# Performance work log

Measured on AMD Instinct MI355X. Metric: run time of the kernel, lower is better.

## Reference

```python
import jax, jax.numpy as jnp
import numpy as np

N0, N1, N2 = 100000, 20000, 4000   # src(block0), dst(block0)=src(block1), dst(block1)
R = 3                               # number of relations
E0, E1 = 160000, 64000              # edges per relation per block
IN_FEATS, HID = 128, 128
TSS, RS = 64, 64
NTOT = 200000                       # global node count for tss/rs embed tables
F_IN = HID + TSS + RS               # IGConv input feature dim = 256


def _lin(key, fi, fo):
    k1, k2 = jax.random.split(key)
    s = float(1.0 / np.sqrt(fi))
    w = jax.random.uniform(k1, (fi, fo), minval=-s, maxval=s, dtype=jnp.float32)
    b = jax.random.uniform(k2, (fo,), minval=-s, maxval=s, dtype=jnp.float32)
    return w, b


def setup_inputs() -> dict:
    ks = jax.random.split(jax.random.key(0), 32)
    inp = {}
    inp["x_user"] = jax.random.normal(ks[0], (N0, IN_FEATS), dtype=jnp.float32)
    inp["tss_embed"] = jax.random.normal(ks[1], (NTOT, TSS), dtype=jnp.float32)
    inp["rs_embed"] = jax.random.normal(ks[2], (NTOT, RS), dtype=jnp.float32)
    inp["src_nid0"] = jax.random.randint(ks[3], (N0,), 0, NTOT)
    inp["src_nid1"] = jax.random.randint(ks[4], (N1,), 0, NTOT)
    inp["e0_src"] = jax.random.randint(ks[5], (R, E0), 0, N0)
    inp["e0_dst"] = jax.random.randint(ks[6], (R, E0), 0, N1)
    inp["e1_src"] = jax.random.randint(ks[7], (R, E1), 0, N1)
    inp["e1_dst"] = jax.random.randint(ks[8], (R, E1), 0, N2)
    inp["embed_w"], inp["embed_b"] = _lin(ks[9], IN_FEATS, HID)
    i = 10
    for l in (1, 2):
        for nm, fi in (("fc1", F_IN), ("fc2", 3 * F_IN), ("fc3", 2 * HID)):
            pw, pb = zip(*[_lin(jax.random.fold_in(ks[i], r), fi, HID) for r in range(R)])
            inp["l%d_%s_w" % (l, nm)] = jnp.stack(pw)  # [R, fi, HID]
            inp["l%d_%s_b" % (l, nm)] = jnp.stack(pb)  # [R, HID]
            i += 1
    inp["attn_w1"], inp["attn_b1"] = _lin(ks[i], HID, HID)
    inp["attn_w2"] = _lin(ks[i + 1], HID, 1)[0]  # Linear(hid,1,bias=False)
    inp["pred_w"], inp["pred_b"] = _lin(ks[i + 2], HID, 1)
    return inp


def _igconv(src_feat, dst_feat, esrc, edst, n_dst, fc1w, fc1b, fc2w, fc2b, fc3w, fc3b):
    # copy_u gather then max/mean/sum segment reductions over destination nodes
    m = src_feat[esrc]                                   # [E, F]
    s = jax.ops.segment_sum(m, edst, num_segments=n_dst)
    deg = jax.ops.segment_sum(jnp.ones(esrc.shape, m.dtype), edst, num_segments=n_dst)
    mean = s / jnp.maximum(deg, 1.0)[:, None]
    mx = jax.ops.segment_max(m, edst, num_segments=n_dst)
    mx = jnp.where(deg[:, None] > 0, mx, jnp.zeros_like(mx))  # DGL zeros for isolated dst
    msg = jnp.concatenate([mx, mean, s], axis=1)         # [n_dst, 3F]
    inp = jnp.concatenate([msg @ fc2w + fc2b, dst_feat @ fc1w + fc1b], axis=1)
    return jax.nn.relu(inp) @ fc3w + fc3b                # [n_dst, HID]


def _attn(z, w1, b1, w2):
    # SemanticAttention: z [N, R, HID]
    w = (jnp.tanh(z @ w1 + b1) @ w2).mean(0)             # [R, 1]
    beta = jax.nn.softmax(w, axis=0)                     # [R, 1]
    return (beta[None] * z).sum(1)                       # [N, HID]


def _forward(x_user, tss_embed, rs_embed, embed_w, embed_b,
             l1_fc1_w, l1_fc1_b, l1_fc2_w, l1_fc2_b, l1_fc3_w, l1_fc3_b,
             l2_fc1_w, l2_fc1_b, l2_fc2_w, l2_fc2_b, l2_fc3_w, l2_fc3_b,
             attn_w1, attn_b1, attn_w2, pred_w, pred_b,
             src_nid0, src_nid1, e0_src, e0_dst, e1_src, e1_dst):
    u0 = x_user @ embed_w + embed_b                      # self.embed
    feat0 = jnp.concatenate([u0, tss_embed[src_nid0], rs_embed[src_nid0]], axis=1)  # [N0,256]
    conv1 = jax.vmap(lambda es, ed, w1, b1, w2, b2, w3, b3:
                     _igconv(feat0, feat0[:N1], es, ed, N1, w1, b1, w2, b2, w3, b3))
    z1 = conv1(e0_src, e0_dst, l1_fc1_w, l1_fc1_b, l1_fc2_w, l1_fc2_b, l1_fc3_w, l1_fc3_b)  # [R,N1,HID]
    h1 = jax.nn.relu(_attn(jnp.transpose(z1, (1, 0, 2)), attn_w1, attn_b1, attn_w2))  # [N1,HID]
    feat1 = jnp.concatenate([h1, tss_embed[src_nid1], rs_embed[src_nid1]], axis=1)    # [N1,256]
    conv2 = jax.vmap(lambda es, ed, w1, b1, w2, b2, w3, b3:
                     _igconv(feat1, feat1[:N2], es, ed, N2, w1, b1, w2, b2, w3, b3))
    z2 = conv2(e1_src, e1_dst, l2_fc1_w, l2_fc1_b, l2_fc2_w, l2_fc2_b, l2_fc3_w, l2_fc3_b)  # [R,N2,HID]
    h2 = _attn(jnp.transpose(z2, (1, 0, 2)), attn_w1, attn_b1, attn_w2)              # [N2,HID]
    return jax.nn.sigmoid(h2 @ pred_w + pred_b)          # [N2,1]


def reference(x_user, tss_embed, rs_embed, src_nid0, src_nid1,
              e0_src, e0_dst, e1_src, e1_dst, embed_w, embed_b,
              l1_fc1_w, l1_fc1_b, l1_fc2_w, l1_fc2_b, l1_fc3_w, l1_fc3_b,
              l2_fc1_w, l2_fc1_b, l2_fc2_w, l2_fc2_b, l2_fc3_w, l2_fc3_b,
              attn_w1, attn_b1, attn_w2, pred_w, pred_b):
    return _forward(x_user, tss_embed, rs_embed, embed_w, embed_b,
                    l1_fc1_w, l1_fc1_b, l1_fc2_w, l1_fc2_b, l1_fc3_w, l1_fc3_b,
                    l2_fc1_w, l2_fc1_b, l2_fc2_w, l2_fc2_b, l2_fc3_w, l2_fc3_b,
                    attn_w1, attn_b1, attn_w2, pred_w, pred_b,
                    src_nid0, src_nid1, e0_src, e0_dst, e1_src, e1_dst)
```

## Files before the change

kernel.cpp:

```cpp
#include <hip/hip_runtime.h>
#include <math.h>


typedef short s16x8 __attribute__((ext_vector_type(8)));
typedef float f32x4 __attribute__((ext_vector_type(4)));

__device__ __forceinline__ ushort f2bf(float f) {
  unsigned u = __float_as_uint(f);
  return (ushort)((u + 0x7FFFu + ((u >> 16) & 1u)) >> 16);
}
__device__ __forceinline__ float bf2f(unsigned hbits) {
  return __uint_as_float(hbits << 16);
}
__device__ __forceinline__ unsigned pack2(float lo, float hi) {
  return (unsigned)f2bf(lo) | ((unsigned)f2bf(hi) << 16);
}

struct PrepAll {
  const float* src[8];
  ushort* dst[8];
  int K[8];
  int total[8];
};

__global__ __launch_bounds__(256) void prep_all(PrepAll P)
{
  int t = blockIdx.z;
  int off = blockIdx.x * 256 + threadIdx.x;
  if (off >= P.total[t]) return;
  int K = P.K[t];
  int k = off % K;
  int n = (off / K) & 127;
  int r = off / (K * 128);
  P.dst[t][off] = f2bf(P.src[t][((size_t)r * K + k) * 128 + n]);
}

struct GemmDesc {
  const void* A; int lda; size_t aStride; int aKind;
  const ushort* Wt; size_t wStride;
  const float* bias; int biasStride;
  void* C; int ldc; size_t cStride; int cKind;
  int M, K, relu;
  const ushort* aggM; const ushort* aggS; const float* invdeg;
  size_t aggStride; int invStride;
  const int* gnid; const float* gtss; const float* grs;
};

__global__ __launch_bounds__(256) void gemm_mfma(GemmDesc d0, GemmDesc d1)
{
  const GemmDesc d = blockIdx.z ? d1 : d0;
  const int r = blockIdx.y;
  __shared__ __align__(16) ushort Bs[2048 * 8];

  const int tid = threadIdx.x;
  const int wave = tid >> 6, lane = tid & 63;
  const int m16 = lane & 15, quad = lane >> 4;
  const int rowBase = blockIdx.x * 64;
  const int row = rowBase + wave * 16 + m16;
  const bool rowOK = row < d.M;
  const ushort* Wt = d.Wt + (size_t)r * d.wStride;

  f32x4 acc[8];
  #pragma unroll
  for (int j = 0; j < 8; ++j)
    #pragma unroll
    for (int p = 0; p < 4; ++p) acc[j][p] = 0.f;

  float idg = 1.f;
  if (d.aKind == 2 && rowOK) idg = d.invdeg[(size_t)r * d.invStride + row];

  const ushort* Ab16 = (const ushort*)d.A + (size_t)r * d.aStride;
  const float*  Ab32 = (const float*)d.A + (size_t)r * d.aStride;

  for (int c0 = 0; c0 < d.K; c0 += 128) {
    if (c0) __syncthreads();
    #pragma unroll
    for (int i = 0; i < 8; ++i) {
      int q = tid + 256 * i;
      int col = ((q >> 6) & 7) * 16 + (q & 15);
      int kk  = c0 + (q >> 9) * 32 + ((q >> 4) & 3) * 8;
      *(uint4*)&Bs[q * 8] = *(const uint4*)(Wt + (size_t)col * d.K + kk);
    }
    __syncthreads();

    #pragma unroll
    for (int ks = 0; ks < 4; ++ks) {
      const int k0 = c0 + ks * 32;
      uint4 pk = make_uint4(0u, 0u, 0u, 0u);
      if (rowOK) {
        if (d.aKind == 1) {
          pk = *(const uint4*)(Ab16 + (size_t)row * d.lda + k0 + quad * 8);
        } else if (d.aKind == 0) {
          float4 fa = *(const float4*)(Ab32 + (size_t)row * d.lda + k0 + quad * 8);
          float4 fb = *(const float4*)(Ab32 + (size_t)row * d.lda + k0 + quad * 8 + 4);
          pk.x = pack2(fa.x, fa.y); pk.y = pack2(fa.z, fa.w);
          pk.z = pack2(fb.x, fb.y); pk.w = pack2(fb.z, fb.w);
        } else {
          int seg = k0 >> 8;
          int jj  = (k0 & 255) + quad * 8;
          const ushort* Ag = (seg == 0 ? d.aggM : d.aggS) + (size_t)r * d.aggStride;
          pk = *(const uint4*)(Ag + (size_t)row * 256 + jj);
          if (seg == 1) {
            pk.x = pack2(bf2f(pk.x & 0xFFFFu) * idg, bf2f(pk.x >> 16) * idg);
            pk.y = pack2(bf2f(pk.y & 0xFFFFu) * idg, bf2f(pk.y >> 16) * idg);
            pk.z = pack2(bf2f(pk.z & 0xFFFFu) * idg, bf2f(pk.z >> 16) * idg);
            pk.w = pack2(bf2f(pk.w & 0xFFFFu) * idg, bf2f(pk.w >> 16) * idg);
          }
        }
      }
      s16x8 af = *(s16x8*)&pk;
      #pragma unroll
      for (int j = 0; j < 8; ++j) {
        s16x8 bf = *(const s16x8*)&Bs[((ks * 8 + j) * 64 + lane) * 8];
        acc[j] = __builtin_amdgcn_mfma_f32_16x16x32_bf16(af, bf, acc[j], 0, 0, 0);
      }
    }
  }

  const float* bias = d.bias + (size_t)r * d.biasStride;
  float bcol[8];
  #pragma unroll
  for (int j = 0; j < 8; ++j) bcol[j] = bias[j * 16 + m16];

  #pragma unroll
  for (int p = 0; p < 4; ++p) {
    int grow = rowBase + wave * 16 + quad * 4 + p;
    if (grow >= d.M) continue;
    if (d.cKind == 0) {
      float* Crow = (float*)d.C + (size_t)r * d.cStride + (size_t)grow * d.ldc;
      #pragma unroll
      for (int j = 0; j < 8; ++j) {
        float v = acc[j][p] + bcol[j];
        if (d.relu) v = fmaxf(v, 0.f);
        Crow[j * 16 + m16] = v;
      }
    } else {
      ushort* Crow = (ushort*)d.C + (size_t)r * d.cStride + (size_t)grow * d.ldc;
      #pragma unroll
      for (int j = 0; j < 8; ++j) {
        float v = acc[j][p] + bcol[j];
        if (d.relu) v = fmaxf(v, 0.f);
        Crow[j * 16 + m16] = f2bf(v);
      }
    }
  }

  if (d.gnid) {
    #pragma unroll
    for (int i = 0; i < 8; ++i) {
      int q = tid + 256 * i;
      int grow = rowBase + (q >> 5);
      int c = q & 31;
      if (grow >= d.M) continue;
      int id = d.gnid[grow];
      float4 v = (c < 16) ? *(const float4*)(d.gtss + (size_t)id * 64 + c * 4)
                          : *(const float4*)(d.grs  + (size_t)id * 64 + (c - 16) * 4);
      uint2 g; g.x = pack2(v.x, v.y); g.y = pack2(v.z, v.w);
      *(uint2*)((ushort*)d.C + (size_t)grow * d.ldc + 128 + c * 4) = g;
    }
  }
}

__global__ __launch_bounds__(256) void attn_mfma(
    const float* __restrict__ z, const ushort* __restrict__ w1t,
    const float* __restrict__ b1, const float* __restrict__ w2,
    int N, float* __restrict__ wsum)
{
  const int r = blockIdx.y;
  const float* zr = z + (size_t)r * N * 128;
  __shared__ __align__(16) ushort Bs[2048 * 8];

  const int tid = threadIdx.x;
  const int wave = tid >> 6, lane = tid & 63;
  const int m16 = lane & 15, quad = lane >> 4;
  const int rowBase = blockIdx.x * 64;
  const int row = rowBase + wave * 16 + m16;
  const bool rowOK = row < N;

  f32x4 acc[8];
  #pragma unroll
  for (int j = 0; j < 8; ++j)
    #pragma unroll
    for (int p = 0; p < 4; ++p) acc[j][p] = 0.f;

  #pragma unroll
  for (int i = 0; i < 8; ++i) {
    int q = tid + 256 * i;
    int col = ((q >> 6) & 7) * 16 + (q & 15);
    int kk  = (q >> 9) * 32 + ((q >> 4) & 3) * 8;
    *(uint4*)&Bs[q * 8] = *(const uint4*)(w1t + (size_t)col * 128 + kk);
  }
  __syncthreads();

  #pragma unroll
  for (int ks = 0; ks < 4; ++ks) {
    const int k0 = ks * 32;
    uint4 pk = make_uint4(0u, 0u, 0u, 0u);
    if (rowOK) {
      float4 fa = *(const float4*)(zr + (size_t)row * 128 + k0 + quad * 8);
      float4 fb = *(const float4*)(zr + (size_t)row * 128 + k0 + quad * 8 + 4);
      pk.x = pack2(fa.x, fa.y); pk.y = pack2(fa.z, fa.w);
      pk.z = pack2(fb.x, fb.y); pk.w = pack2(fb.z, fb.w);
    }
    s16x8 af = *(s16x8*)&pk;
    #pragma unroll
    for (int j = 0; j < 8; ++j) {
      s16x8 bf = *(const s16x8*)&Bs[((ks * 8 + j) * 64 + lane) * 8];
      acc[j] = __builtin_amdgcn_mfma_f32_16x16x32_bf16(af, bf, acc[j], 0, 0, 0);
    }
  }

  float b1c[8], w2c[8];
  #pragma unroll
  for (int j = 0; j < 8; ++j) { b1c[j] = b1[j * 16 + m16]; w2c[j] = w2[j * 16 + m16]; }

  float local = 0.f;
  #pragma unroll
  for (int p = 0; p < 4; ++p) {
    int grow = rowBase + wave * 16 + quad * 4 + p;
    if (grow >= N) continue;
    #pragma unroll
    for (int j = 0; j < 8; ++j)
      local += tanhf(acc[j][p] + b1c[j]) * w2c[j];
  }
  #pragma unroll
  for (int o = 32; o > 0; o >>= 1) local += __shfl_down(local, o);
  __shared__ float red[4];
  if (lane == 0) red[wave] = local;
  __syncthreads();
  if (tid == 0) atomicAdd(&wsum[r], red[0] + red[1] + red[2] + red[3]);
}

__global__ void count_deg(const int* __restrict__ edst, int E, int N, int* __restrict__ deg)
{
  int e = blockIdx.x * blockDim.x + threadIdx.x;
  int r = blockIdx.y;
  if (e < E) atomicAdd(&deg[r * N + edst[(size_t)r * E + e]], 1);
}

__global__ __launch_bounds__(1024) void scan_kernel(
    const int* __restrict__ deg, int* __restrict__ rowptr,
    int* __restrict__ cursor, int N)
{
  __shared__ int wtot[16];
  __shared__ int chunk_total_s;
  const int tid = threadIdx.x, lane = tid & 63, wid = tid >> 6;
  int running = 0;
  for (int base = 0; base < N; base += 4096) {
    int i0 = base + tid * 4;
    int d0 = 0, d1 = 0, d2 = 0, d3 = 0;
    if (i0 < N) {
      if (i0 + 3 < N) { int4 t = *(const int4*)(deg + i0); d0 = t.x; d1 = t.y; d2 = t.z; d3 = t.w; }
      else { d0 = deg[i0]; if (i0+1 < N) d1 = deg[i0+1]; if (i0+2 < N) d2 = deg[i0+2]; }
    }
    int tsum = d0 + d1 + d2 + d3;
    int incl = tsum;
    #pragma unroll
    for (int o = 1; o < 64; o <<= 1) {
      int t = __shfl_up(incl, o);
      if (lane >= o) incl += t;
    }
    if (lane == 63) wtot[wid] = incl;
    __syncthreads();
    if (wid == 0 && lane < 16) {
      int t = wtot[lane];
      int inc = t;
      #pragma unroll
      for (int o = 1; o < 16; o <<= 1) {
        int u = __shfl_up(inc, o);
        if (lane >= o) inc += u;
      }
      wtot[lane] = inc - t;
      if (lane == 15) chunk_total_s = inc;
    }
    __syncthreads();
    int excl = running + wtot[wid] + (incl - tsum);
    if (i0 < N) {
      int e1 = excl + d0, e2 = e1 + d1, e3 = e2 + d2;
      if (i0 + 3 < N) {
        *(int4*)(rowptr + i0) = make_int4(excl, e1, e2, e3);
        *(int4*)(cursor + i0) = make_int4(0, 0, 0, 0);
      } else {
        rowptr[i0] = excl; cursor[i0] = 0;
        if (i0+1 < N) { rowptr[i0+1] = e1; cursor[i0+1] = 0; }
        if (i0+2 < N) { rowptr[i0+2] = e2; cursor[i0+2] = 0; }
      }
    }
    running += chunk_total_s;
    __syncthreads();
  }
  if (tid == 0) rowptr[N] = running;
}

__global__ void fill_csr(const int* __restrict__ esrc, const int* __restrict__ edst,
                         int E, int N, const int* __restrict__ rowptr,
                         int* __restrict__ cursor, int* __restrict__ csr)
{
  int e = blockIdx.x * blockDim.x + threadIdx.x;
  int r = blockIdx.y;
  if (e >= E) return;
  int d = r * N + edst[(size_t)r * E + e];
  int pos = atomicAdd(&cursor[d], 1);
  csr[rowptr[d] + pos] = esrc[(size_t)r * E + e];
}

__global__ __launch_bounds__(256) void agg_kernel(
    const ushort* __restrict__ feat, const int* __restrict__ csr,
    const int* __restrict__ rowptr, int N, int c0, int cr, int CH,
    ushort* __restrict__ aggS, ushort* __restrict__ aggM, float* __restrict__ invdeg)
{
  const int wid = threadIdx.x >> 6, lane = threadIdx.x & 63;
  const int node = blockIdx.x * 4 + wid;
  if (node >= cr) return;
  const int g = blockIdx.y * N + c0 + node;
  const int o = blockIdx.y * CH + node;
  const int start = rowptr[g], end = rowptr[g + 1];
  const int j = lane * 4;
  float s0 = 0.f, s1 = 0.f, s2 = 0.f, s3 = 0.f;
  float m0 = -INFINITY, m1 = -INFINITY, m2 = -INFINITY, m3 = -INFINITY;
  int e = start;
  for (; e + 4 <= end; e += 4) {
    int sa = csr[e], sb = csr[e+1], sc = csr[e+2], sd = csr[e+3];
    uint2 va = *(const uint2*)(feat + (size_t)sa * 256 + j);
    uint2 vb = *(const uint2*)(feat + (size_t)sb * 256 + j);
    uint2 vc = *(const uint2*)(feat + (size_t)sc * 256 + j);
    uint2 vd = *(const uint2*)(feat + (size_t)sd * 256 + j);
    float a0, a1, a2, a3;
    a0 = bf2f(va.x & 0xFFFFu); a1 = bf2f(va.x >> 16); a2 = bf2f(va.y & 0xFFFFu); a3 = bf2f(va.y >> 16);
    s0 += a0; s1 += a1; s2 += a2; s3 += a3;
    m0 = fmaxf(m0, a0); m1 = fmaxf(m1, a1); m2 = fmaxf(m2, a2); m3 = fmaxf(m3, a3);
    a0 = bf2f(vb.x & 0xFFFFu); a1 = bf2f(vb.x >> 16); a2 = bf2f(vb.y & 0xFFFFu); a3 = bf2f(vb.y >> 16);
    s0 += a0; s1 += a1; s2 += a2; s3 += a3;
    m0 = fmaxf(m0, a0); m1 = fmaxf(m1, a1); m2 = fmaxf(m2, a2); m3 = fmaxf(m3, a3);
    a0 = bf2f(vc.x & 0xFFFFu); a1 = bf2f(vc.x >> 16); a2 = bf2f(vc.y & 0xFFFFu); a3 = bf2f(vc.y >> 16);
    s0 += a0; s1 += a1; s2 += a2; s3 += a3;
    m0 = fmaxf(m0, a0); m1 = fmaxf(m1, a1); m2 = fmaxf(m2, a2); m3 = fmaxf(m3, a3);
    a0 = bf2f(vd.x & 0xFFFFu); a1 = bf2f(vd.x >> 16); a2 = bf2f(vd.y & 0xFFFFu); a3 = bf2f(vd.y >> 16);
    s0 += a0; s1 += a1; s2 += a2; s3 += a3;
    m0 = fmaxf(m0, a0); m1 = fmaxf(m1, a1); m2 = fmaxf(m2, a2); m3 = fmaxf(m3, a3);
  }
  for (; e < end; ++e) {
    int src = csr[e];
    uint2 v = *(const uint2*)(feat + (size_t)src * 256 + j);
    float a0 = bf2f(v.x & 0xFFFFu), a1 = bf2f(v.x >> 16);
    float a2 = bf2f(v.y & 0xFFFFu), a3 = bf2f(v.y >> 16);
    s0 += a0; s1 += a1; s2 += a2; s3 += a3;
    m0 = fmaxf(m0, a0); m1 = fmaxf(m1, a1); m2 = fmaxf(m2, a2); m3 = fmaxf(m3, a3);
  }
  if (end == start) { m0 = m1 = m2 = m3 = 0.f; }
  uint2 ps; ps.x = pack2(s0, s1); ps.y = pack2(s2, s3);
  *(uint2*)(aggS + (size_t)o * 256 + j) = ps;
  uint2 pm; pm.x = pack2(m0, m1); pm.y = pack2(m2, m3);
  *(uint2*)(aggM + (size_t)o * 256 + j) = pm;
  if (lane == 0) invdeg[o] = 1.f / fmaxf((float)(end - start), 1.f);
}

__global__ void beta_kernel(const float* __restrict__ wsum, float invN, float* __restrict__ beta) {
  float w0 = wsum[0] * invN, w1 = wsum[1] * invN, w2 = wsum[2] * invN;
  float m  = fmaxf(w0, fmaxf(w1, w2));
  float e0 = expf(w0 - m), e1 = expf(w1 - m), e2 = expf(w2 - m);
  float s  = e0 + e1 + e2;
  beta[0] = e0 / s; beta[1] = e1 / s; beta[2] = e2 / s;
}

__global__ __launch_bounds__(256) void combine1_kernel(
    const float* __restrict__ z1, const float* __restrict__ beta,
    const float* __restrict__ tss, const float* __restrict__ rs,
    const int* __restrict__ nid, int N, ushort* __restrict__ feat1)
{
  int n = blockIdx.x, t = threadIdx.x;
  size_t NH = (size_t)N * 128;
  if (t < 128) {
    float v = beta[0] * z1[(size_t)n*128 + t] + beta[1] * z1[NH + (size_t)n*128 + t]
            + beta[2] * z1[2*NH + (size_t)n*128 + t];
    feat1[(size_t)n*256 + t] = f2bf(fmaxf(v, 0.f));
  } else {
    int j = t - 128;
    int id = nid[n];
    float v = (j < 64) ? tss[(size_t)id*64 + j] : rs[(size_t)id*64 + j - 64];
    feat1[(size_t)n*256 + t] = f2bf(v);
  }
}

__global__ __launch_bounds__(128) void combine2_pred(
    const float* __restrict__ z2, const float* __restrict__ beta, int N,
    const float* __restrict__ pw, const float* __restrict__ pb, float* __restrict__ out)
{
  int n = blockIdx.x, t = threadIdx.x;
  size_t NH = (size_t)N * 128;
  float h = beta[0] * z2[(size_t)n*128 + t] + beta[1] * z2[NH + (size_t)n*128 + t]
          + beta[2] * z2[2*NH + (size_t)n*128 + t];
  float p = h * pw[t];
  #pragma unroll
  for (int o = 32; o > 0; o >>= 1) p += __shfl_down(p, o);
  __shared__ float red[2];
  if ((t & 63) == 0) red[t >> 6] = p;
  __syncthreads();
  if (t == 0) {
    float v = red[0] + red[1] + pb[0];
    out[n] = 1.f / (1.f + expf(-v));
  }
}

extern "C" void kernel_launch(void* const* d_in, const int* in_sizes, int n_in,
                              void* d_out, int out_size, void* d_ws, size_t ws_size,
                              hipStream_t stream)
{
  const float* x_user  = (const float*)d_in[0];
  const float* tss     = (const float*)d_in[1];
  const float* rs      = (const float*)d_in[2];
  const int* src_nid0  = (const int*)d_in[3];
  const int* src_nid1  = (const int*)d_in[4];
  const int* e0_src    = (const int*)d_in[5];
  const int* e0_dst    = (const int*)d_in[6];
  const int* e1_src    = (const int*)d_in[7];
  const int* e1_dst    = (const int*)d_in[8];
  const float* embed_w = (const float*)d_in[9];
  const float* embed_b = (const float*)d_in[10];
  const float* l1w[3]  = {(const float*)d_in[11], (const float*)d_in[13], (const float*)d_in[15]};
  const float* l1b[3]  = {(const float*)d_in[12], (const float*)d_in[14], (const float*)d_in[16]};
  const float* l2w[3]  = {(const float*)d_in[17], (const float*)d_in[19], (const float*)d_in[21]};
  const float* l2b[3]  = {(const float*)d_in[18], (const float*)d_in[20], (const float*)d_in[22]};
  const float* attn_w1 = (const float*)d_in[23];
  const float* attn_b1 = (const float*)d_in[24];
  const float* attn_w2 = (const float*)d_in[25];
  const float* pred_w  = (const float*)d_in[26];
  const float* pred_b  = (const float*)d_in[27];
  float* out = (float*)d_out;

  const int N0 = in_sizes[0] / 128;
  const int N1 = in_sizes[4];
  const int N2 = out_size;
  const int E0 = in_sizes[5] / 3;
  const int E1 = in_sizes[7] / 3;

  char* wp = (char*)d_ws;
  auto walloc = [&](size_t bytes) {
    char* p = wp; wp += (bytes + 255) & ~(size_t)255; return p;
  };
  ushort* feat0  = (ushort*)walloc((size_t)N0 * 256 * 2);
  ushort* inp    = (ushort*)walloc((size_t)3 * N1 * 256 * 2);
  float*  z      = (float*)walloc((size_t)3 * N1 * 128 * 4);
  ushort* wt_emb = (ushort*)walloc((size_t)128 * 128 * 2);
  ushort* wt_attn = (ushort*)walloc((size_t)128 * 128 * 2);
  ushort* wt_fc1[2], *wt_fc2[2], *wt_fc3[2];
  for (int l = 0; l < 2; ++l) {
    wt_fc1[l] = (ushort*)walloc((size_t)3 * 256 * 128 * 2);
    wt_fc2[l] = (ushort*)walloc((size_t)3 * 768 * 128 * 2);
    wt_fc3[l] = (ushort*)walloc((size_t)3 * 256 * 128 * 2);
  }
  int*   degcnt = (int*)walloc((size_t)3 * N1 * 4);
  int*   rowptr = (int*)walloc((size_t)(3 * N1 + 1) * 4);
  int*   csr    = (int*)walloc((size_t)3 * E0 * 4);
  float* small  = (float*)walloc(256);
  float* wsum = small;
  float* beta = small + 4;
  ushort* feat1 = feat0;

  size_t used = (size_t)(wp - (char*)d_ws);
  size_t avail = (ws_size > used + 65536) ? (ws_size - used - 65536) : 0;
  const size_t per_row = (size_t)3 * (2 * 256 * 2 + 4 + 64);
  int CH = (int)(avail / per_row);
  if (CH > N1) CH = N1;
  if (CH < 1024) CH = 1024;
  ushort* aggS   = (ushort*)walloc((size_t)3 * CH * 256 * 2);
  ushort* aggM   = (ushort*)walloc((size_t)3 * CH * 256 * 2);
  float*  invdeg = (float*)walloc((size_t)3 * CH * 4);
  (void)n_in;

  {
    PrepAll P;
    P.src[0] = embed_w;  P.dst[0] = wt_emb;    P.K[0] = 128; P.total[0] = 128 * 128;
    P.src[1] = attn_w1;  P.dst[1] = wt_attn;   P.K[1] = 128; P.total[1] = 128 * 128;
    P.src[2] = l1w[0];   P.dst[2] = wt_fc1[0]; P.K[2] = 256; P.total[2] = 3 * 256 * 128;
    P.src[3] = l1w[1];   P.dst[3] = wt_fc2[0]; P.K[3] = 768; P.total[3] = 3 * 768 * 128;
    P.src[4] = l1w[2];   P.dst[4] = wt_fc3[0]; P.K[4] = 256; P.total[4] = 3 * 256 * 128;
    P.src[5] = l2w[0];   P.dst[5] = wt_fc1[1]; P.K[5] = 256; P.total[5] = 3 * 256 * 128;
    P.src[6] = l2w[1];   P.dst[6] = wt_fc2[1]; P.K[6] = 768; P.total[6] = 3 * 768 * 128;
    P.src[7] = l2w[2];   P.dst[7] = wt_fc3[1]; P.K[7] = 256; P.total[7] = 3 * 256 * 128;
    prep_all<<<dim3((3 * 768 * 128 + 255) / 256, 1, 8), 256, 0, stream>>>(P);
  }

  GemmDesc dz = {};

  {
    GemmDesc d{};
    d.A = x_user; d.lda = 128; d.aStride = 0; d.aKind = 0;
    d.Wt = wt_emb; d.wStride = 0; d.bias = embed_b; d.biasStride = 0;
    d.C = feat0; d.ldc = 256; d.cStride = 0; d.cKind = 1;
    d.M = N0; d.K = 128; d.relu = 0;
    d.aggM = aggM; d.aggS = aggS; d.invdeg = invdeg; d.aggStride = 0; d.invStride = 0;
    d.gnid = src_nid0; d.gtss = tss; d.grs = rs;
    gemm_mfma<<<dim3((N0 + 63) / 64, 1, 1), 256, 0, stream>>>(d, dz);
  }

  for (int layer = 0; layer < 2; ++layer) {
    const ushort* featS = layer ? feat1 : feat0;
    int Nd = layer ? N2 : N1;
    int E  = layer ? E1 : E0;
    const int* es = layer ? e1_src : e0_src;
    const int* ed = layer ? e1_dst : e0_dst;
    const float* const* lb = layer ? l2b : l1b;

    hipMemsetAsync(degcnt, 0, (size_t)3 * Nd * 4, stream);
    count_deg<<<dim3((E + 255) / 256, 3), 256, 0, stream>>>(ed, E, Nd, degcnt);
    scan_kernel<<<1, 1024, 0, stream>>>(degcnt, rowptr, degcnt, 3 * Nd);
    fill_csr<<<dim3((E + 255) / 256, 3), 256, 0, stream>>>(es, ed, E, Nd, rowptr, degcnt, csr);

    for (int c0 = 0; c0 < Nd; c0 += CH) {
      int cr = (Nd - c0 < CH) ? (Nd - c0) : CH;
      agg_kernel<<<dim3((cr + 3) / 4, 3), 256, 0, stream>>>(
          featS, csr, rowptr, Nd, c0, cr, CH, aggS, aggM, invdeg);
      GemmDesc d2{};
      d2.A = nullptr; d2.lda = 0; d2.aStride = 0; d2.aKind = 2;
      d2.Wt = wt_fc2[layer]; d2.wStride = (size_t)768 * 128; d2.bias = lb[1]; d2.biasStride = 128;
      d2.C = inp + (size_t)c0 * 256; d2.ldc = 256; d2.cStride = (size_t)Nd * 256; d2.cKind = 1;
      d2.M = cr; d2.K = 768; d2.relu = 1;
      d2.aggM = aggM; d2.aggS = aggS; d2.invdeg = invdeg;
      d2.aggStride = (size_t)CH * 256; d2.invStride = CH;
      GemmDesc d1{};
      d1.A = featS + (size_t)c0 * 256; d1.lda = 256; d1.aStride = 0; d1.aKind = 1;
      d1.Wt = wt_fc1[layer]; d1.wStride = (size_t)256 * 128; d1.bias = lb[0]; d1.biasStride = 128;
      d1.C = inp + 128 + (size_t)c0 * 256; d1.ldc = 256; d1.cStride = (size_t)Nd * 256; d1.cKind = 1;
      d1.M = cr; d1.K = 256; d1.relu = 1;
      d1.aggM = aggM; d1.aggS = aggS; d1.invdeg = invdeg; d1.aggStride = 0; d1.invStride = 0;
      gemm_mfma<<<dim3((cr + 63) / 64, 3, 2), 256, 0, stream>>>(d2, d1);
    }
    {
      GemmDesc d3{};
      d3.A = inp; d3.lda = 256; d3.aStride = (size_t)N1 * 0 + (size_t)Nd * 256; d3.aKind = 1;
      d3.Wt = wt_fc3[layer]; d3.wStride = (size_t)256 * 128; d3.bias = lb[2]; d3.biasStride = 128;
      d3.C = z; d3.ldc = 128; d3.cStride = (size_t)Nd * 128; d3.cKind = 0;
      d3.M = Nd; d3.K = 256; d3.relu = 0;
      d3.aggM = aggM; d3.aggS = aggS; d3.invdeg = invdeg; d3.aggStride = 0; d3.invStride = 0;
      gemm_mfma<<<dim3((Nd + 63) / 64, 3, 1), 256, 0, stream>>>(d3, dz);
    }

    hipMemsetAsync(wsum, 0, 3 * sizeof(float), stream);
    attn_mfma<<<dim3((Nd + 63) / 64, 3), 256, 0, stream>>>(z, wt_attn, attn_b1, attn_w2, Nd, wsum);
    beta_kernel<<<1, 1, 0, stream>>>(wsum, 1.0f / (float)Nd, beta);

    if (layer == 0) {
      combine1_kernel<<<N1, 256, 0, stream>>>(z, beta, tss, rs, src_nid1, N1, feat1);
    } else {
      combine2_pred<<<N2, 128, 0, stream>>>(z, beta, N2, pred_w, pred_b, out);
    }
  }
}
```

Before: 546.8 us.

## Template GEMM on K and A-kind, halve LDS tile, prefetch A fragments

The GEMM kernel is specialised by a template on K and on how A is loaded, which removes the runtime branches on aKind. The shared-memory B tile shrinks from 128 to 64 K-columns per stage, halving LDS use so more blocks fit per CU, and launch bounds now request 4 blocks per SM. A fragments are loaded into registers ahead of the B staging: all of them up front when K is at most 256, otherwise per chunk. The attention kernel gets the same change. The cost is more __syncthreads barriers and higher register pressure from the prefetched fragments.

```diff
diff --git a/kernel.cpp b/kernel.cpp
--- a/kernel.cpp
+++ b/kernel.cpp
@@ -46,11 +46,42 @@
   const int* gnid; const float* gtss; const float* grs;
 };
 
-__global__ __launch_bounds__(256) void gemm_mfma(GemmDesc d0, GemmDesc d1)
-{
-  const GemmDesc d = blockIdx.z ? d1 : d0;
-  const int r = blockIdx.y;
-  __shared__ __align__(16) ushort Bs[2048 * 8];
+template<int AKIND>
+__device__ __forceinline__ uint4 loadA(const void* Ab, const ushort* AgM,
+                                       const ushort* AgS, int lda, int row,
+                                       bool rowOK, int k0, int quad, float idg)
+{
+  uint4 pk = make_uint4(0u, 0u, 0u, 0u);
+  if (rowOK) {
+    if constexpr (AKIND == 1) {
+      pk = *(const uint4*)((const ushort*)Ab + (size_t)row * lda + k0 + quad * 8);
+    } else if constexpr (AKIND == 0) {
+      const float* A32 = (const float*)Ab;
+      float4 fa = *(const float4*)(A32 + (size_t)row * lda + k0 + quad * 8);
+      float4 fb = *(const float4*)(A32 + (size_t)row * lda + k0 + quad * 8 + 4);
+      pk.x = pack2(fa.x, fa.y); pk.y = pack2(fa.z, fa.w);
+      pk.z = pack2(fb.x, fb.y); pk.w = pack2(fb.z, fb.w);
+    } else {
+      int seg = k0 >> 8;
+      int jj  = (k0 & 255) + quad * 8;
+      const ushort* Ag = (seg == 0) ? AgM : AgS;
+      pk = *(const uint4*)(Ag + (size_t)row * 256 + jj);
+      if (seg == 1) {
+        pk.x = pack2(bf2f(pk.x & 0xFFFFu) * idg, bf2f(pk.x >> 16) * idg);
+        pk.y = pack2(bf2f(pk.y & 0xFFFFu) * idg, bf2f(pk.y >> 16) * idg);
+        pk.z = pack2(bf2f(pk.z & 0xFFFFu) * idg, bf2f(pk.z >> 16) * idg);
+        pk.w = pack2(bf2f(pk.w & 0xFFFFu) * idg, bf2f(pk.w >> 16) * idg);
+      }
+    }
+  }
+  return pk;
+}
+
+template<int K, int AKIND>
+__device__ __forceinline__ void gemm_core(const GemmDesc& d, int r, ushort* Bs)
+{
+  constexpr int NC = K / 64;
+  constexpr int NF = K / 32;
 
   const int tid = threadIdx.x;
   const int wave = tid >> 6, lane = tid & 63;
@@ -60,54 +91,46 @@
   const bool rowOK = row < d.M;
   const ushort* Wt = d.Wt + (size_t)r * d.wStride;
 
+  const void* Ab = (const char*)d.A +
+      (size_t)r * d.aStride * (AKIND == 0 ? sizeof(float) : sizeof(ushort));
+  const ushort* AgM = d.aggM + (size_t)r * d.aggStride;
+  const ushort* AgS = d.aggS + (size_t)r * d.aggStride;
+
+  float idg = 1.f;
+  if (AKIND == 2 && rowOK) idg = d.invdeg[(size_t)r * d.invStride + row];
+
   f32x4 acc[8];
   #pragma unroll
   for (int j = 0; j < 8; ++j)
     #pragma unroll
     for (int p = 0; p < 4; ++p) acc[j][p] = 0.f;
 
-  float idg = 1.f;
-  if (d.aKind == 2 && rowOK) idg = d.invdeg[(size_t)r * d.invStride + row];
-
-  const ushort* Ab16 = (const ushort*)d.A + (size_t)r * d.aStride;
-  const float*  Ab32 = (const float*)d.A + (size_t)r * d.aStride;
-
-  for (int c0 = 0; c0 < d.K; c0 += 128) {
-    if (c0) __syncthreads();
-    #pragma unroll
-    for (int i = 0; i < 8; ++i) {
+  uint4 pkAll[(K <= 256) ? NF : 2];
+  if constexpr (K <= 256) {
+    #pragma unroll
+    for (int f = 0; f < NF; ++f)
+      pkAll[f] = loadA<AKIND>(Ab, AgM, AgS, d.lda, row, rowOK, f * 32, quad, idg);
+  }
+
+  #pragma unroll
+  for (int c = 0; c < NC; ++c) {
+    if constexpr (K > 256) {
+      pkAll[0] = loadA<AKIND>(Ab, AgM, AgS, d.lda, row, rowOK, c * 64,      quad, idg);
+      pkAll[1] = loadA<AKIND>(Ab, AgM, AgS, d.lda, row, rowOK, c * 64 + 32, quad, idg);
+    }
+    if (c) __syncthreads();
+    #pragma unroll
+    for (int i = 0; i < 4; ++i) {
       int q = tid + 256 * i;
       int col = ((q >> 6) & 7) * 16 + (q & 15);
-      int kk  = c0 + (q >> 9) * 32 + ((q >> 4) & 3) * 8;
-      *(uint4*)&Bs[q * 8] = *(const uint4*)(Wt + (size_t)col * d.K + kk);
+      int kk  = c * 64 + (q >> 9) * 32 + ((q >> 4) & 3) * 8;
+      *(uint4*)&Bs[q * 8] = *(const uint4*)(Wt + (size_t)col * K + kk);
     }
     __syncthreads();
 
     #pragma unroll
-    for (int ks = 0; ks < 4; ++ks) {
-      const int k0 = c0 + ks * 32;
-      uint4 pk = make_uint4(0u, 0u, 0u, 0u);
-      if (rowOK) {
-        if (d.aKind == 1) {
-          pk = *(const uint4*)(Ab16 + (size_t)row * d.lda + k0 + quad * 8);
-        } else if (d.aKind == 0) {
-          float4 fa = *(const float4*)(Ab32 + (size_t)row * d.lda + k0 + quad * 8);
-          float4 fb = *(const float4*)(Ab32 + (size_t)row * d.lda + k0 + quad * 8 + 4);
-          pk.x = pack2(fa.x, fa.y); pk.y = pack2(fa.z, fa.w);
-          pk.z = pack2(fb.x, fb.y); pk.w = pack2(fb.z, fb.w);
-        } else {
-          int seg = k0 >> 8;
-          int jj  = (k0 & 255) + quad * 8;
-          const ushort* Ag = (seg == 0 ? d.aggM : d.aggS) + (size_t)r * d.aggStride;
-          pk = *(const uint4*)(Ag + (size_t)row * 256 + jj);
-          if (seg == 1) {
-            pk.x = pack2(bf2f(pk.x & 0xFFFFu) * idg, bf2f(pk.x >> 16) * idg);
-            pk.y = pack2(bf2f(pk.y & 0xFFFFu) * idg, bf2f(pk.y >> 16) * idg);
-            pk.z = pack2(bf2f(pk.z & 0xFFFFu) * idg, bf2f(pk.z >> 16) * idg);
-            pk.w = pack2(bf2f(pk.w & 0xFFFFu) * idg, bf2f(pk.w >> 16) * idg);
-          }
-        }
-      }
+    for (int ks = 0; ks < 2; ++ks) {
+      uint4 pk = (K <= 256) ? pkAll[c * 2 + ks] : pkAll[ks];
       s16x8 af = *(s16x8*)&pk;
       #pragma unroll
       for (int j = 0; j < 8; ++j) {
@@ -145,30 +168,42 @@
     }
   }
 
-  if (d.gnid) {
-    #pragma unroll
-    for (int i = 0; i < 8; ++i) {
-      int q = tid + 256 * i;
-      int grow = rowBase + (q >> 5);
-      int c = q & 31;
-      if (grow >= d.M) continue;
-      int id = d.gnid[grow];
-      float4 v = (c < 16) ? *(const float4*)(d.gtss + (size_t)id * 64 + c * 4)
-                          : *(const float4*)(d.grs  + (size_t)id * 64 + (c - 16) * 4);
-      uint2 g; g.x = pack2(v.x, v.y); g.y = pack2(v.z, v.w);
-      *(uint2*)((ushort*)d.C + (size_t)grow * d.ldc + 128 + c * 4) = g;
-    }
-  }
-}
-
-__global__ __launch_bounds__(256) void attn_mfma(
+  if constexpr (K == 128) {
+    if (d.gnid) {
+      #pragma unroll
+      for (int i = 0; i < 8; ++i) {
+        int q = tid + 256 * i;
+        int grow = rowBase + (q >> 5);
+        int c = q & 31;
+        if (grow >= d.M) continue;
+        int id = d.gnid[grow];
+        float4 v = (c < 16) ? *(const float4*)(d.gtss + (size_t)id * 64 + c * 4)
+                            : *(const float4*)(d.grs  + (size_t)id * 64 + (c - 16) * 4);
+        uint2 g; g.x = pack2(v.x, v.y); g.y = pack2(v.z, v.w);
+        *(uint2*)((ushort*)d.C + (size_t)grow * d.ldc + 128 + c * 4) = g;
+      }
+    }
+  }
+}
+
+__global__ __launch_bounds__(256, 4) void gemm_mfma(GemmDesc d0, GemmDesc d1)
+{
+  __shared__ __align__(16) ushort Bs[1024 * 8];
+  const GemmDesc& d = blockIdx.z ? d1 : d0;
+  const int r = blockIdx.y;
+  if (d.K == 128)      gemm_core<128, 0>(d, r, Bs);
+  else if (d.K == 256) gemm_core<256, 1>(d, r, Bs);
+  else                 gemm_core<768, 2>(d, r, Bs);
+}
+
+__global__ __launch_bounds__(256, 4) void attn_mfma(
     const float* __restrict__ z, const ushort* __restrict__ w1t,
     const float* __restrict__ b1, const float* __restrict__ w2,
     int N, float* __restrict__ wsum)
 {
   const int r = blockIdx.y;
   const float* zr = z + (size_t)r * N * 128;
-  __shared__ __align__(16) ushort Bs[2048 * 8];
+  __shared__ __align__(16) ushort Bs[1024 * 8];
 
   const int tid = threadIdx.x;
   const int wave = tid >> 6, lane = tid & 63;
@@ -183,30 +218,39 @@
     #pragma unroll
     for (int p = 0; p < 4; ++p) acc[j][p] = 0.f;
 
-  #pragma unroll
-  for (int i = 0; i < 8; ++i) {
-    int q = tid + 256 * i;
-    int col = ((q >> 6) & 7) * 16 + (q & 15);
-    int kk  = (q >> 9) * 32 + ((q >> 4) & 3) * 8;
-    *(uint4*)&Bs[q * 8] = *(const uint4*)(w1t + (size_t)col * 128 + kk);
-  }
-  __syncthreads();
-
-  #pragma unroll
-  for (int ks = 0; ks < 4; ++ks) {
-    const int k0 = ks * 32;
+  uint4 pkAll[4];
+  #pragma unroll
+  for (int f = 0; f < 4; ++f) {
     uint4 pk = make_uint4(0u, 0u, 0u, 0u);
     if (rowOK) {
-      float4 fa = *(const float4*)(zr + (size_t)row * 128 + k0 + quad * 8);
-      float4 fb = *(const float4*)(zr + (size_t)row * 128 + k0 + quad * 8 + 4);
+      float4 fa = *(const float4*)(zr + (size_t)row * 128 + f * 32 + quad * 8);
+      float4 fb = *(const float4*)(zr + (size_t)row * 128 + f * 32 + quad * 8 + 4);
       pk.x = pack2(fa.x, fa.y); pk.y = pack2(fa.z, fa.w);
       pk.z = pack2(fb.x, fb.y); pk.w = pack2(fb.z, fb.w);
     }
-    s16x8 af = *(s16x8*)&pk;
-    #pragma unroll
-    for (int j = 0; j < 8; ++j) {
-      s16x8 bf = *(const s16x8*)&Bs[((ks * 8 + j) * 64 + lane) * 8];
-      acc[j] = __builtin_amdgcn_mfma_f32_16x16x32_bf16(af, bf, acc[j], 0, 0, 0);
+    pkAll[f] = pk;
+  }
+
+  #pragma unroll
+  for (int c = 0; c < 2; ++c) {
+    if (c) __syncthreads();
+    #pragma unroll
+    for (int i = 0; i < 4; ++i) {
+      int q = tid + 256 * i;
+      int col = ((q >> 6) & 7) * 16 + (q & 15);
+      int kk  = c * 64 + (q >> 9) * 32 + ((q >> 4) & 3) * 8;
+      *(uint4*)&Bs[q * 8] = *(const uint4*)(w1t + (size_t)col * 128 + kk);
+    }
+    __syncthreads();
+
+    #pragma unroll
+    for (int ks = 0; ks < 2; ++ks) {
+      s16x8 af = *(s16x8*)&pkAll[c * 2 + ks];
+      #pragma unroll
+      for (int j = 0; j < 8; ++j) {
+        s16x8 bf = *(const s16x8*)&Bs[((ks * 8 + j) * 64 + lane) * 8];
+        acc[j] = __builtin_amdgcn_mfma_f32_16x16x32_bf16(af, bf, acc[j], 0, 0, 0);
+      }
     }
   }
 
@@ -482,6 +526,7 @@
   }
 
   GemmDesc dz = {};
+  dz.K = 256;
 
   {
     GemmDesc d{};
@@ -528,7 +573,7 @@
     }
     {
       GemmDesc d3{};
-      d3.A = inp; d3.lda = 256; d3.aStride = (size_t)N1 * 0 + (size_t)Nd * 256; d3.aKind = 1;
+      d3.A = inp; d3.lda = 256; d3.aStride = (size_t)Nd * 256; d3.aKind = 1;
       d3.Wt = wt_fc3[layer]; d3.wStride = (size_t)256 * 128; d3.bias = lb[2]; d3.biasStride = 128;
       d3.C = z; d3.ldc = 128; d3.cStride = (size_t)Nd * 128; d3.cKind = 0;
       d3.M = Nd; d3.K = 256; d3.relu = 0;
```

Result: no change. 551.1 us (+0.8%).
